# Performance work log

Measured on AMD Instinct MI355X. Metric: run time of the kernel, lower is better.

Reference implementation:

```python
import jax, jax.numpy as jnp
import numpy as np

B = 262144
D = 16          # input_dim
D2 = D // 2     # 8, == hidden_dim
H = 8           # hidden_dim
L = 15          # num_layers (couplings)
NH = 3          # hidden_block_layers
EPS = 1e-6
SLOPE = 0.01    # LeakyReLU default


def setup_inputs() -> dict:
    key = jax.random.key(0)
    ks = jax.random.split(key, 8)
    z = jax.random.normal(ks[0], (B, D), dtype=jnp.float32)
    s = 0.2  # keep log_s away from the +/-5 clamp saturation
    W_in = jax.random.normal(ks[1], (L, 2, D2, H), dtype=jnp.float32) * s
    b_in = jax.random.normal(ks[2], (L, 2, H), dtype=jnp.float32) * s
    W_hid = jax.random.normal(ks[3], (L, 2, NH, H, H), dtype=jnp.float32) * s
    b_hid = jax.random.normal(ks[4], (L, 2, NH, H), dtype=jnp.float32) * s
    W_out = jax.random.normal(ks[5], (L, 2, H, D2), dtype=jnp.float32) * s
    b_out = jax.random.normal(ks[6], (L, 2, D2), dtype=jnp.float32) * s
    # 14 random permutations between couplings + identity after the last coupling
    rng = np.random.default_rng(0)
    perms = np.stack([rng.permutation(D) for _ in range(L - 1)] + [np.arange(D)])
    perms = jnp.asarray(perms, dtype=jnp.int32)  # [L, D]
    return {"z": z, "W_in": W_in, "b_in": b_in, "W_hid": W_hid,
            "b_hid": b_hid, "W_out": W_out, "b_out": b_out, "perms": perms}


def _mlp(x, Wi, bi, Wh, bh, Wo, bo):
    # LinearBlock: (Linear+LeakyReLU) + NH x (Linear+LeakyReLU) + Linear
    h = jax.nn.leaky_relu(x @ Wi + bi, SLOPE)
    for j in range(NH):  # NH is a small static constant
        h = jax.nn.leaky_relu(h @ Wh[j] + bh[j], SLOPE)
    return h @ Wo + bo


def _flow(z, W_in, b_in, W_hid, b_hid, W_out, b_out, perms):
    def step(carry, params):
        z, ld = carry
        Wi, bi, Wh, bh, Wo, bo, perm = params
        z_l, z_r = z[:, :D2], z[:, D2:]
        log_s = jnp.clip(_mlp(z_l, Wi[0], bi[0], Wh[0], bh[0], Wo[0], bo[0]), -5.0, 5.0)
        b = _mlp(z_l, Wi[1], bi[1], Wh[1], bh[1], Wo[1], bo[1])
        y_r = (jnp.exp(log_s) + EPS) * z_r + b
        y = jnp.concatenate([z_l, y_r], axis=1)
        ld = ld + jnp.sum(log_s, axis=1)
        y = y[:, perm]  # Permutation layer (identity for the last step)
        return (y, ld), None

    ld0 = jnp.zeros(z.shape[0], dtype=z.dtype)
    (y, ld), _ = jax.lax.scan(step, (z, ld0), (W_in, b_in, W_hid, b_hid, W_out, b_out, perms))
    return y, ld


def reference(z, W_in, b_in, W_hid, b_hid, W_out, b_out, perms):
    return _flow(z, W_in, b_in, W_hid, b_hid, W_out, b_out, perms)
```

## Files before the change

### kernel.cpp

```cpp
#include <hip/hip_runtime.h>

#define BN 262144
#define HALF (BN / 2)
#define LNUM 15
#define NSTG 151
#define NF4 (NSTG * 18)
#define LOG2E 1.4426950408889634f
#define LN2 0.6931471805599453f
#define L2CLIP 7.2134752044448170f

extern "C" __global__ void build_slab(
    const float* __restrict__ Wi, const float* __restrict__ bi,
    const float* __restrict__ Wh, const float* __restrict__ bh,
    const float* __restrict__ Wo, const float* __restrict__ bo,
    float* __restrict__ slab) {
    int idx = blockIdx.x * 256 + threadIdx.x;
    if (idx >= NSTG * 72) return;
    int sl = idx / 72, k = idx % 72;
    if (sl == NSTG - 1) sl = 0;
    const int l = sl / 10, r = sl % 10, net = r / 5, st = r % 5;
    const int nb = l * 2 + net;
    const float sc = (net == 0 && st == 4) ? LOG2E : 1.0f;
    float v;
    if (k < 8) {
        if (st == 0)      v = bi[nb * 8 + k];
        else if (st < 4)  v = bh[(nb * 3 + (st - 1)) * 8 + k];
        else              v = bo[nb * 8 + k] * sc;
    } else {
        const int kk = k - 8;
        if (st == 0)      v = Wi[nb * 64 + kk];
        else if (st < 4)  v = Wh[(nb * 3 + (st - 1)) * 64 + kk];
        else              v = Wo[nb * 64 + kk] * sc;
    }
    slab[idx] = v;
}

extern "C" __global__ void compose_perms(const int* __restrict__ perms, int* __restrict__ c) {
    if (threadIdx.x != 0 || blockIdx.x != 0) return;
    int cur[16];
    for (int j = 0; j < 16; ++j) { cur[j] = j; c[j] = j; }
    for (int l = 0; l < LNUM; ++l) {
        int nx[16];
        for (int j = 0; j < 16; ++j) nx[j] = cur[perms[l * 16 + j]];
        for (int j = 0; j < 16; ++j) { c[(l + 1) * 16 + j] = nx[j]; cur[j] = nx[j]; }
    }
}

#define GB(gb, k) ((k) % 4 == 0 ? gb[(k) / 4].x : (k) % 4 == 1 ? gb[(k) / 4].y \
                 : (k) % 4 == 2 ? gb[(k) / 4].z : gb[(k) / 4].w)

#define CHA(IN, OUT, BUF)                                                     \
    {                                                                         \
        _Pragma("unroll") for (int o = 0; o < 8; ++o) {                       \
            const float bb = GB(BUF, o);                                      \
            const float w0 = GB(BUF, 8 + o), w1 = GB(BUF, 16 + o);            \
            _Pragma("unroll") for (int s = 0; s < 2; ++s)                     \
                OUT[s][o] = fmaf(IN[s][1], w1, fmaf(IN[s][0], w0, bb));       \
        }                                                                     \
        _Pragma("unroll") for (int j = 0; j < 6; ++j) BUF[j] = gptr[j];       \
        gptr += 6;                                                            \
        __builtin_amdgcn_sched_barrier(0);                                    \
    }
#define CHB(IN, OUT, BUF)                                                     \
    {                                                                         \
        _Pragma("unroll") for (int o = 0; o < 8; ++o) {                       \
            const float w2 = GB(BUF, o), w3 = GB(BUF, 8 + o), w4 = GB(BUF, 16 + o); \
            _Pragma("unroll") for (int s = 0; s < 2; ++s)                     \
                OUT[s][o] = fmaf(IN[s][4], w4,                                 \
                             fmaf(IN[s][3], w3, fmaf(IN[s][2], w2, OUT[s][o]))); \
        }                                                                     \
        _Pragma("unroll") for (int j = 0; j < 6; ++j) BUF[j] = gptr[j];       \
        gptr += 6;                                                            \
        __builtin_amdgcn_sched_barrier(0);                                    \
    }
#define CHC(IN, OUT, BUF, DOLR)                                               \
    {                                                                         \
        _Pragma("unroll") for (int o = 0; o < 8; ++o) {                       \
            const float w5 = GB(BUF, o), w6 = GB(BUF, 8 + o), w7 = GB(BUF, 16 + o); \
            _Pragma("unroll") for (int s = 0; s < 2; ++s) {                   \
                float a = fmaf(IN[s][7], w7,                                   \
                            fmaf(IN[s][6], w6, fmaf(IN[s][5], w5, OUT[s][o]))); \
                OUT[s][o] = (DOLR) ? fmaxf(a, 0.01f * a) : a;                 \
            }                                                                 \
        }                                                                     \
        _Pragma("unroll") for (int j = 0; j < 6; ++j) BUF[j] = gptr[j];       \
        gptr += 6;                                                            \
        __builtin_amdgcn_sched_barrier(0);                                    \
    }
#define STG(IN, OUT, DOLR) CHA(IN, OUT, B0) CHB(IN, OUT, B1) CHC(IN, OUT, B2, DOLR)

extern "C" __global__ void __launch_bounds__(512) flow_fwd(
    const float* __restrict__ z, const float* __restrict__ slab,
    const int* __restrict__ cperm,
    float* __restrict__ outy, float* __restrict__ outld) {
    __shared__ float4 wls[NF4];
    __shared__ float xs[512 * 33];
    const int t = threadIdx.x;
    const long i = (long)blockIdx.x * 512 + t;
    float* __restrict__ myx = &xs[t * 33];

    {
        const float4* gs = reinterpret_cast<const float4*>(slab);
        for (int k = t; k < NF4; k += 512) wls[k] = gs[k];
    }
    {
        const float4* zp = reinterpret_cast<const float4*>(z + i * 16);
        const float4* zq = reinterpret_cast<const float4*>(z + (i + HALF) * 16);
#pragma unroll
        for (int q = 0; q < 4; ++q) {
            float4 a = zp[q], b = zq[q];
            myx[4 * q] = a.x; myx[4 * q + 1] = a.y; myx[4 * q + 2] = a.z; myx[4 * q + 3] = a.w;
            myx[16 + 4 * q] = b.x; myx[17 + 4 * q] = b.y; myx[18 + 4 * q] = b.z; myx[19 + 4 * q] = b.w;
        }
    }
    float ld2A = 0.f, ld2B = 0.f;
    __syncthreads();

    float4 B0[6], B1[6], B2[6];
#pragma unroll
    for (int j = 0; j < 6; ++j) { B0[j] = wls[j]; B1[j] = wls[6 + j]; B2[j] = wls[12 + j]; }
    const float4* gptr = wls + 18;
    __builtin_amdgcn_sched_barrier(0);

#pragma unroll 1
    for (int l = 0; l < LNUM; ++l) {
        const int* __restrict__ cl = cperm + l * 16;
        float in2[2][8];
#pragma unroll
        for (int j = 0; j < 8; ++j) {
            const int off = cl[j];
            in2[0][j] = myx[off];
            in2[1][j] = myx[16 + off];
        }
        float h[2][8], g[2][8], sf[2][8], bf[2][8];
        STG(in2, h, 1) STG(h, g, 1) STG(g, h, 1) STG(h, g, 1) STG(g, sf, 0)
        STG(in2, h, 1) STG(h, g, 1) STG(g, h, 1) STG(h, g, 1) STG(g, bf, 0)

#pragma unroll
        for (int k = 0; k < 8; ++k) {
            const int off = cl[8 + k];
            const float cA = fminf(fmaxf(sf[0][k], -L2CLIP), L2CLIP);
            const float cB = fminf(fmaxf(sf[1][k], -L2CLIP), L2CLIP);
            ld2A += cA; ld2B += cB;
            myx[off]      = fmaf(__builtin_amdgcn_exp2f(cA) + 1e-6f, myx[off],      bf[0][k]);
            myx[16 + off] = fmaf(__builtin_amdgcn_exp2f(cB) + 1e-6f, myx[16 + off], bf[1][k]);
        }
    }

    {
        const int* __restrict__ cf = cperm + LNUM * 16;
        float4 oa[4], ob[4];
#pragma unroll
        for (int q = 0; q < 4; ++q) {
            const int c0 = cf[4 * q], c1 = cf[4 * q + 1], c2 = cf[4 * q + 2], c3 = cf[4 * q + 3];
            oa[q].x = myx[c0]; oa[q].y = myx[c1]; oa[q].z = myx[c2]; oa[q].w = myx[c3];
            ob[q].x = myx[16 + c0]; ob[q].y = myx[16 + c1];
            ob[q].z = myx[16 + c2]; ob[q].w = myx[16 + c3];
        }
        float4* ya = reinterpret_cast<float4*>(outy + i * 16);
        float4* yb = reinterpret_cast<float4*>(outy + (i + HALF) * 16);
#pragma unroll
        for (int q = 0; q < 4; ++q) { ya[q] = oa[q]; yb[q] = ob[q]; }
        outld[i] = ld2A * LN2;
        outld[i + HALF] = ld2B * LN2;
    }
}

extern "C" void kernel_launch(void* const* d_in, const int* in_sizes, int n_in,
                              void* d_out, int out_size, void* d_ws, size_t ws_size,
                              hipStream_t stream) {
    const float* z = (const float*)d_in[0];
    const float* Wi = (const float*)d_in[1];
    const float* bi = (const float*)d_in[2];
    const float* Wh = (const float*)d_in[3];
    const float* bh = (const float*)d_in[4];
    const float* Wo = (const float*)d_in[5];
    const float* bo = (const float*)d_in[6];
    const int* perms = (const int*)d_in[7];
    float* out = (float*)d_out;
    float* slab = (float*)d_ws;
    int* cperm = (int*)(slab + NSTG * 72);

    hipLaunchKernelGGL(build_slab, dim3((NSTG * 72 + 255) / 256), dim3(256), 0, stream,
                       Wi, bi, Wh, bh, Wo, bo, slab);
    hipLaunchKernelGGL(compose_perms, dim3(1), dim3(64), 0, stream, perms, cperm);
    hipLaunchKernelGGL(flow_fwd, dim3(HALF / 512), dim3(512), 0, stream,
                       z, slab, cperm, out, out + (size_t)BN * 16);
}
```

Baseline: 95.93 us.

## Split weight slab into LDS-streamed and scalar-loaded parts per stage

Reorganises the per-stage weight slab into two regions. The bias and the first three input rows (32 floats) are read as uniform scalar loads straight from global memory. The remaining 40 floats are staged in LDS and double-buffered across stages (WA/WB). This reduces LDS footprint and LDS read traffic per stage and shifts part of the weight fetching onto the scalar memory path. The risk is scalar-load latency and extra register pressure from the 10-float4 prefetch buffers.

```diff
diff --git a/kernel.cpp b/kernel.cpp
--- a/kernel.cpp
+++ b/kernel.cpp
@@ -4,35 +4,50 @@
 #define HALF (BN / 2)
 #define LNUM 15
 #define NSTG 151
-#define NF4 (NSTG * 18)
+#define NL4 (NSTG * 10)
+#define NLF (NSTG * 40)
+#define NSF (NSTG * 32)
 #define LOG2E 1.4426950408889634f
 #define LN2 0.6931471805599453f
 #define L2CLIP 7.2134752044448170f
+
+typedef __attribute__((ext_vector_type(4))) float f4;
+
+__device__ __forceinline__ float raw_val(
+    const float* Wi, const float* bi, const float* Wh, const float* bh,
+    const float* Wo, const float* bo, int sl, int k ) {
+    const int l = sl / 10, r = sl % 10, net = r / 5, st = r % 5;
+    const int nb = l * 2 + net;
+    const float sc = (net == 0 && st == 4) ? LOG2E : 1.0f;
+    if (k < 8) {
+        if (st == 0)      return bi[nb * 8 + k];
+        else if (st < 4)  return bh[(nb * 3 + (st - 1)) * 8 + k];
+        else              return bo[nb * 8 + k] * sc;
+    } else {
+        const int kk = k - 8;
+        if (st == 0)      return Wi[nb * 64 + kk];
+        else if (st < 4)  return Wh[(nb * 3 + (st - 1)) * 64 + kk];
+        else              return Wo[nb * 64 + kk] * sc;
+    }
+}
 
 extern "C" __global__ void build_slab(
     const float* __restrict__ Wi, const float* __restrict__ bi,
     const float* __restrict__ Wh, const float* __restrict__ bh,
     const float* __restrict__ Wo, const float* __restrict__ bo,
-    float* __restrict__ slab) {
+    float* __restrict__ ws) {
     int idx = blockIdx.x * 256 + threadIdx.x;
-    if (idx >= NSTG * 72) return;
-    int sl = idx / 72, k = idx % 72;
-    if (sl == NSTG - 1) sl = 0;
-    const int l = sl / 10, r = sl % 10, net = r / 5, st = r % 5;
-    const int nb = l * 2 + net;
-    const float sc = (net == 0 && st == 4) ? LOG2E : 1.0f;
-    float v;
-    if (k < 8) {
-        if (st == 0)      v = bi[nb * 8 + k];
-        else if (st < 4)  v = bh[(nb * 3 + (st - 1)) * 8 + k];
-        else              v = bo[nb * 8 + k] * sc;
+    if (idx >= NLF + NSF) return;
+    if (idx < NLF) {
+        int sl = idx / 40, j = idx % 40;
+        if (sl == NSTG - 1) sl = 0;
+        ws[idx] = raw_val(Wi, bi, Wh, bh, Wo, bo, sl, 32 + j);
     } else {
-        const int kk = k - 8;
-        if (st == 0)      v = Wi[nb * 64 + kk];
-        else if (st < 4)  v = Wh[(nb * 3 + (st - 1)) * 64 + kk];
-        else              v = Wo[nb * 64 + kk] * sc;
-    }
-    slab[idx] = v;
+        const int q = idx - NLF;
+        int sl = q / 32, j = q % 32;
+        if (sl == NSTG - 1) sl = 0;
+        ws[idx] = raw_val(Wi, bi, Wh, bh, Wo, bo, sl, j);
+    }
 }
 
 extern "C" __global__ void compose_perms(const int* __restrict__ perms, int* __restrict__ c) {
@@ -46,62 +61,56 @@
     }
 }
 
-#define GB(gb, k) ((k) % 4 == 0 ? gb[(k) / 4].x : (k) % 4 == 1 ? gb[(k) / 4].y \
-                 : (k) % 4 == 2 ? gb[(k) / 4].z : gb[(k) / 4].w)
-
-#define CHA(IN, OUT, BUF)                                                     \
+#define GBX(W, k) (W[(k) / 4][(k) % 4])
+
+#define PREFL(PB, SIDX)                                                       \
     {                                                                         \
+        const f4* sp = &wlds[(SIDX) * 10];                                    \
+        _Pragma("unroll") for (int j = 0; j < 10; ++j) PB[j] = sp[j];         \
+        __builtin_amdgcn_sched_barrier(0);                                    \
+    }
+
+#define STGH(IN, OUT, DOLR, PB, PIDX, CB, WS)                                 \
+    {                                                                         \
+        PREFL(PB, PIDX)                                                       \
         _Pragma("unroll") for (int o = 0; o < 8; ++o) {                       \
-            const float bb = GB(BUF, o);                                      \
-            const float w0 = GB(BUF, 8 + o), w1 = GB(BUF, 16 + o);            \
+            const float bb = (WS)[o], w0 = (WS)[8 + o];                       \
             _Pragma("unroll") for (int s = 0; s < 2; ++s)                     \
-                OUT[s][o] = fmaf(IN[s][1], w1, fmaf(IN[s][0], w0, bb));       \
+                OUT[s][o] = fmaf(IN[s][0], w0, bb);                           \
         }                                                                     \
-        _Pragma("unroll") for (int j = 0; j < 6; ++j) BUF[j] = gptr[j];       \
-        gptr += 6;                                                            \
-        __builtin_amdgcn_sched_barrier(0);                                    \
-    }
-#define CHB(IN, OUT, BUF)                                                     \
-    {                                                                         \
-        _Pragma("unroll") for (int o = 0; o < 8; ++o) {                       \
-            const float w2 = GB(BUF, o), w3 = GB(BUF, 8 + o), w4 = GB(BUF, 16 + o); \
+        _Pragma("unroll") for (int i2 = 1; i2 < 3; ++i2)                      \
+            _Pragma("unroll") for (int o = 0; o < 8; ++o) {                   \
+                const float w = (WS)[8 + i2 * 8 + o];                         \
+                _Pragma("unroll") for (int s = 0; s < 2; ++s)                 \
+                    OUT[s][o] = fmaf(IN[s][i2], w, OUT[s][o]);                \
+            }                                                                 \
+        _Pragma("unroll") for (int rr = 0; rr < 5; ++rr)                      \
+            _Pragma("unroll") for (int o = 0; o < 8; ++o) {                   \
+                const float w = GBX(CB, rr * 8 + o);                          \
+                _Pragma("unroll") for (int s = 0; s < 2; ++s)                 \
+                    OUT[s][o] = fmaf(IN[s][3 + rr], w, OUT[s][o]);            \
+            }                                                                 \
+        if (DOLR) {                                                           \
             _Pragma("unroll") for (int s = 0; s < 2; ++s)                     \
-                OUT[s][o] = fmaf(IN[s][4], w4,                                 \
-                             fmaf(IN[s][3], w3, fmaf(IN[s][2], w2, OUT[s][o]))); \
+                _Pragma("unroll") for (int o = 0; o < 8; ++o)                 \
+                    OUT[s][o] = fmaxf(OUT[s][o], 0.01f * OUT[s][o]);          \
         }                                                                     \
-        _Pragma("unroll") for (int j = 0; j < 6; ++j) BUF[j] = gptr[j];       \
-        gptr += 6;                                                            \
-        __builtin_amdgcn_sched_barrier(0);                                    \
-    }
-#define CHC(IN, OUT, BUF, DOLR)                                               \
-    {                                                                         \
-        _Pragma("unroll") for (int o = 0; o < 8; ++o) {                       \
-            const float w5 = GB(BUF, o), w6 = GB(BUF, 8 + o), w7 = GB(BUF, 16 + o); \
-            _Pragma("unroll") for (int s = 0; s < 2; ++s) {                   \
-                float a = fmaf(IN[s][7], w7,                                   \
-                            fmaf(IN[s][6], w6, fmaf(IN[s][5], w5, OUT[s][o]))); \
-                OUT[s][o] = (DOLR) ? fmaxf(a, 0.01f * a) : a;                 \
-            }                                                                 \
-        }                                                                     \
-        _Pragma("unroll") for (int j = 0; j < 6; ++j) BUF[j] = gptr[j];       \
-        gptr += 6;                                                            \
-        __builtin_amdgcn_sched_barrier(0);                                    \
-    }
-#define STG(IN, OUT, DOLR) CHA(IN, OUT, B0) CHB(IN, OUT, B1) CHC(IN, OUT, B2, DOLR)
+    }
 
 extern "C" __global__ void __launch_bounds__(512) flow_fwd(
-    const float* __restrict__ z, const float* __restrict__ slab,
+    const float* __restrict__ z, const float* __restrict__ ws,
     const int* __restrict__ cperm,
     float* __restrict__ outy, float* __restrict__ outld) {
-    __shared__ float4 wls[NF4];
+    __shared__ f4 wlds[NL4];
     __shared__ float xs[512 * 33];
     const int t = threadIdx.x;
     const long i = (long)blockIdx.x * 512 + t;
     float* __restrict__ myx = &xs[t * 33];
+    const float* __restrict__ gsm = ws + NLF;
 
     {
-        const float4* gs = reinterpret_cast<const float4*>(slab);
-        for (int k = t; k < NF4; k += 512) wls[k] = gs[k];
+        const f4* gs = reinterpret_cast<const f4*>(ws);
+        for (int k = t; k < NL4; k += 512) wlds[k] = gs[k];
     }
     {
         const float4* zp = reinterpret_cast<const float4*>(z + i * 16);
@@ -116,15 +125,14 @@
     float ld2A = 0.f, ld2B = 0.f;
     __syncthreads();
 
-    float4 B0[6], B1[6], B2[6];
-#pragma unroll
-    for (int j = 0; j < 6; ++j) { B0[j] = wls[j]; B1[j] = wls[6 + j]; B2[j] = wls[12 + j]; }
-    const float4* gptr = wls + 18;
-    __builtin_amdgcn_sched_barrier(0);
+    f4 WA[10], WB[10];
+    PREFL(WA, 0)
 
 #pragma unroll 1
     for (int l = 0; l < LNUM; ++l) {
         const int* __restrict__ cl = cperm + l * 16;
+        const float* __restrict__ wsm = gsm + l * 320;
+        const int base = l * 10;
         float in2[2][8];
 #pragma unroll
         for (int j = 0; j < 8; ++j) {
@@ -133,8 +141,16 @@
             in2[1][j] = myx[16 + off];
         }
         float h[2][8], g[2][8], sf[2][8], bf[2][8];
-        STG(in2, h, 1) STG(h, g, 1) STG(g, h, 1) STG(h, g, 1) STG(g, sf, 0)
-        STG(in2, h, 1) STG(h, g, 1) STG(g, h, 1) STG(h, g, 1) STG(g, bf, 0)
+        STGH(in2, h, 1, WB, base + 1, WA, wsm + 0)
+        STGH(h, g, 1,   WA, base + 2, WB, wsm + 32)
+        STGH(g, h, 1,   WB, base + 3, WA, wsm + 64)
+        STGH(h, g, 1,   WA, base + 4, WB, wsm + 96)
+        STGH(g, sf, 0,  WB, base + 5, WA, wsm + 128)
+        STGH(in2, h, 1, WA, base + 6, WB, wsm + 160)
+        STGH(h, g, 1,   WB, base + 7, WA, wsm + 192)
+        STGH(g, h, 1,   WA, base + 8, WB, wsm + 224)
+        STGH(h, g, 1,   WB, base + 9, WA, wsm + 256)
+        STGH(g, bf, 0,  WA, base + 10, WB, wsm + 288)
 
 #pragma unroll
         for (int k = 0; k < 8; ++k) {
@@ -178,12 +194,12 @@
     const float* bo = (const float*)d_in[6];
     const int* perms = (const int*)d_in[7];
     float* out = (float*)d_out;
-    float* slab = (float*)d_ws;
-    int* cperm = (int*)(slab + NSTG * 72);
-
-    hipLaunchKernelGGL(build_slab, dim3((NSTG * 72 + 255) / 256), dim3(256), 0, stream,
-                       Wi, bi, Wh, bh, Wo, bo, slab);
+    float* ws = (float*)d_ws;
+    int* cperm = (int*)(ws + NLF + NSF);
+
+    hipLaunchKernelGGL(build_slab, dim3((NLF + NSF + 255) / 256), dim3(256), 0, stream,
+                       Wi, bi, Wh, bh, Wo, bo, ws);
     hipLaunchKernelGGL(compose_perms, dim3(1), dim3(64), 0, stream, perms, cperm);
     hipLaunchKernelGGL(flow_fwd, dim3(HALF / 512), dim3(512), 0, stream,
-                       z, slab, cperm, out, out + (size_t)BN * 16);
-}
+                       z, ws, cperm, out, out + (size_t)BN * 16);
+}
```

Measured after the change: 139.7 us. 45.7% more time.
